# Performance work log

Hardware: AMD Instinct MI355X
Metric: run time of the kernel (lower is better)

## Reference

```python
import jax, jax.numpy as jnp
import numpy as np

N = 50000   # nodes
E = 800000  # edges
IN, HID, OUT, H = 128, 256, 128, 4
C1 = HID // H  # per-head channels for conv1/conv2
EPS_LN = 1e-5


def layer_norm(x, g, b):
    mu = x.mean(-1, keepdims=True)
    var = ((x - mu) ** 2).mean(-1, keepdims=True)
    return (x - mu) * jax.lax.rsqrt(var + EPS_LN) * g + b


def gatv2(x, src, dst, edge_attr, Wl, bl, Wr, br, We, att, bias, heads, ch, n):
    # PyG GATv2Conv (concat=True, negative_slope=0.2, share_weights=False)
    xl = (x @ Wl + bl).reshape(-1, heads, ch)   # [N,H,C] source transform
    xr = (x @ Wr + br).reshape(-1, heads, ch)   # [N,H,C] target transform
    e = (edge_attr @ We).reshape(-1, heads, ch) # [E,H,C] edge transform (no bias)
    m = jax.nn.leaky_relu(xl[src] + xr[dst] + e, 0.2)     # [E,H,C]
    logits = jnp.einsum('ehc,hc->eh', m, att)             # [E,H]
    mx = jax.ops.segment_max(logits, dst, num_segments=n) # segment softmax over dst
    a = jnp.exp(logits - mx[dst])
    denom = jax.ops.segment_sum(a, dst, num_segments=n)
    alpha = a / (denom[dst] + 1e-16)                      # [E,H]
    out = jax.ops.segment_sum(xl[src] * alpha[..., None], dst, num_segments=n)
    return out.reshape(-1, heads * ch) + bias


def setup_inputs() -> dict:
    key = jax.random.key(0)
    ks = jax.random.split(key, 24)
    s = 0.05
    inp = {
        'x': jax.random.normal(ks[0], (N, IN), jnp.float32),
        'edge_index': jax.random.randint(ks[1], (2, E), 0, N, jnp.int32),
        'edge_attr': jax.random.uniform(ks[2], (E, 1), jnp.float32),
        # conv1: in=IN, out per head=C1, heads=H
        'Wl1': jax.random.normal(ks[3], (IN, HID)) * s,  'bl1': jnp.zeros((HID,)),
        'Wr1': jax.random.normal(ks[4], (IN, HID)) * s,  'br1': jnp.zeros((HID,)),
        'We1': jax.random.normal(ks[5], (1, HID)) * s,
        'att1': jax.random.normal(ks[6], (H, C1)) * s,   'bo1': jnp.zeros((HID,)),
        'g1': jnp.ones((HID,)), 'be1': jnp.zeros((HID,)),
        # conv2: in=HID
        'Wl2': jax.random.normal(ks[7], (HID, HID)) * s, 'bl2': jnp.zeros((HID,)),
        'Wr2': jax.random.normal(ks[8], (HID, HID)) * s, 'br2': jnp.zeros((HID,)),
        'We2': jax.random.normal(ks[9], (1, HID)) * s,
        'att2': jax.random.normal(ks[10], (H, C1)) * s,  'bo2': jnp.zeros((HID,)),
        'g2': jnp.ones((HID,)), 'be2': jnp.zeros((HID,)),
        # conv3: heads=1, out=OUT
        'Wl3': jax.random.normal(ks[11], (HID, OUT)) * s, 'bl3': jnp.zeros((OUT,)),
        'Wr3': jax.random.normal(ks[12], (HID, OUT)) * s, 'br3': jnp.zeros((OUT,)),
        'We3': jax.random.normal(ks[13], (1, OUT)) * s,
        'att3': jax.random.normal(ks[14], (1, OUT)) * s,  'bo3': jnp.zeros((OUT,)),
        'g3': jnp.ones((OUT,)), 'be3': jnp.zeros((OUT,)),
    }
    return inp


def reference(x, edge_index, edge_attr,
              Wl1, bl1, Wr1, br1, We1, att1, bo1, g1, be1,
              Wl2, bl2, Wr2, br2, We2, att2, bo2, g2, be2,
              Wl3, bl3, Wr3, br3, We3, att3, bo3, g3, be3):
    src, dst = edge_index[0], edge_index[1]
    h = gatv2(x, src, dst, edge_attr, Wl1, bl1, Wr1, br1, We1, att1, bo1, H, C1, N)
    h = jax.nn.elu(layer_norm(h, g1, be1))  # dropout inactive at inference
    h = gatv2(h, src, dst, edge_attr, Wl2, bl2, Wr2, br2, We2, att2, bo2, H, C1, N)
    h = jax.nn.elu(layer_norm(h, g2, be2))
    h = gatv2(h, src, dst, edge_attr, Wl3, bl3, Wr3, br3, We3, att3, bo3, 1, OUT, N)
    return layer_norm(h, g3, be3)
```

## Files before the change

kernel.cpp:

```cpp
#include <hip/hip_runtime.h>
#include <cstdint>
#include <cstddef>

typedef unsigned short u16;
typedef __attribute__((ext_vector_type(8))) short short8v;
typedef __attribute__((ext_vector_type(4))) float f32x4;

#define IN_DIM 128
#define HID_DIM 256
#define OUT_DIM 128
#define HEADS 4

__device__ __forceinline__ float b2f(u16 v) {
    return __uint_as_float(((unsigned)v) << 16);
}
__device__ __forceinline__ u16 f2b(float f) {
    unsigned u = __float_as_uint(f);
    u += 0x7fffu + ((u >> 16) & 1u);
    return (u16)(u >> 16);
}


__global__ void count_k(const int* __restrict__ dst, int* __restrict__ counts, int ne) {
    int i = blockIdx.x * blockDim.x + threadIdx.x;
    if (i < ne) atomicAdd(&counts[dst[i]], 1);
}

__global__ __launch_bounds__(1024) void scan_k(const int* __restrict__ counts,
                                               int* __restrict__ offs,
                                               int* __restrict__ cursor, int n) {
    __shared__ int wtot[16];
    __shared__ int carry_s;
    int tid = threadIdx.x, wv = tid >> 6, ln = tid & 63;
    if (tid == 0) carry_s = 0;
    __syncthreads();
    for (int base = 0; base < n; base += 4096) {
        int i0 = base + tid * 4;
        int4 c4 = {0, 0, 0, 0};
        if (i0 + 3 < n) c4 = *(const int4*)(counts + i0);
        else {
            if (i0     < n) c4.x = counts[i0];
            if (i0 + 1 < n) c4.y = counts[i0 + 1];
            if (i0 + 2 < n) c4.z = counts[i0 + 2];
            if (i0 + 3 < n) c4.w = counts[i0 + 3];
        }
        int s0 = c4.x, s1 = s0 + c4.y, s2 = s1 + c4.z, s3 = s2 + c4.w;
        int v = s3;
#pragma unroll
        for (int o = 1; o < 64; o <<= 1) {
            int t = __shfl_up(v, o);
            if (ln >= o) v += t;
        }
        if (ln == 63) wtot[wv] = v;
        int wpref = v - s3;
        __syncthreads();
        if (wv == 0) {
            int w2 = (ln < 16) ? wtot[ln] : 0;
#pragma unroll
            for (int o = 1; o < 16; o <<= 1) {
                int t = __shfl_up(w2, o);
                if (ln >= o) w2 += t;
            }
            if (ln < 16) wtot[ln] = w2;
        }
        __syncthreads();
        int wbase = carry_s + (wv ? wtot[wv - 1] : 0);
        int ex0 = wbase + wpref;
        if (i0     < n) { offs[i0]     = ex0;      cursor[i0]     = ex0; }
        if (i0 + 1 < n) { offs[i0 + 1] = ex0 + s0; cursor[i0 + 1] = ex0 + s0; }
        if (i0 + 2 < n) { offs[i0 + 2] = ex0 + s1; cursor[i0 + 2] = ex0 + s1; }
        if (i0 + 3 < n) { offs[i0 + 3] = ex0 + s2; cursor[i0 + 3] = ex0 + s2; }
        __syncthreads();
        if (tid == 0) carry_s += wtot[15];
        __syncthreads();
    }
    if (threadIdx.x == 0) offs[n] = carry_s;
}

__global__ void fill_k(const int* __restrict__ src, const int* __restrict__ dst,
                       const float* __restrict__ ea, int* __restrict__ cursor,
                       int2* __restrict__ cedge, int ne) {
    int i = blockIdx.x * blockDim.x + threadIdx.x;
    if (i < ne) {
        int p = atomicAdd(&cursor[dst[i]], 1);
        int2 t;
        t.x = src[i];
        t.y = __float_as_int(ea[i]);
        cedge[p] = t;
    }
}


template <int KG>
__global__ void xpack_k(const float* __restrict__ X, short* __restrict__ Xp, int total) {
    int gid = blockIdx.x * blockDim.x + threadIdx.x;
    if (gid >= total) return;
    int lane = gid & 63;
    int kg = (gid >> 6) % KG;
    int rt = gid / (64 * KG);
    int row = rt * 16 + (lane & 15);
    int k0 = kg * 32 + ((lane >> 4) << 3);
    const float* src = X + (size_t)row * (KG * 32) + k0;
    short8v o;
#pragma unroll
    for (int j = 0; j < 8; j++) o[j] = (short)f2b(src[j]);
    ((short8v*)Xp)[gid] = o;
}

template <int K, int HOUT>
__global__ void packw_k(const float* __restrict__ Wl, const float* __restrict__ Wr,
                        short* __restrict__ Wp) {
    constexpr int KG = K / 32;
    int gid = blockIdx.x * blockDim.x + threadIdx.x;
    int lane = gid & 63;
    int kg = (gid >> 6) % KG;
    int nt = gid / (64 * KG);
    int col = nt * 16 + (lane & 15);
    int k0 = kg * 32 + ((lane >> 4) << 3);
    const float* Wsrc = (col < HOUT) ? Wl : Wr;
    int c2 = (col < HOUT) ? col : col - HOUT;
    short8v o;
#pragma unroll
    for (int j = 0; j < 8; j++) o[j] = (short)f2b(Wsrc[(size_t)(k0 + j) * HOUT + c2]);
    ((short8v*)Wp)[gid] = o;
}


template <int KG, int NT, int HOUT, int R>
__global__ __launch_bounds__(256) void gemm_mfma(
    const short* __restrict__ Xp, const short* __restrict__ Wp,
    const float* __restrict__ bl, const float* __restrict__ br,
    u16* __restrict__ XL, u16* __restrict__ XR, int nrt) {
    constexpr int NCG = NT / 8;
    int w = threadIdx.x >> 6, lane = threadIdx.x & 63;
    int cg = blockIdx.x % NCG;
    int rt0 = (blockIdx.x / NCG) * R;
    if (rt0 >= nrt) return;
    int rcnt = min(R, nrt - rt0);
    int nt0 = cg * 8 + w * 2;
    const short8v* wb = (const short8v*)Wp + lane;
    short8v wf0[KG], wf1[KG];
#pragma unroll
    for (int kg = 0; kg < KG; kg++) {
        wf0[kg] = wb[(size_t)(nt0 * KG + kg) * 64];
        wf1[kg] = wb[(size_t)((nt0 + 1) * KG + kg) * 64];
    }
    int colg0 = nt0 * 16 + ((lane >> 4) << 2);
    int colg1 = colg0 + 16;
    bool isr0 = colg0 >= HOUT;
    bool isr1 = colg1 >= HOUT;
    int cl0 = colg0 - (isr0 ? HOUT : 0);
    int cl1 = colg1 - (isr1 ? HOUT : 0);
    float4 bb0 = *(const float4*)((isr0 ? br : bl) + cl0);
    float4 bb1 = *(const float4*)((isr1 ? br : bl) + cl1);
    u16* ob0 = (isr0 ? XR : XL) + cl0;
    u16* ob1 = (isr1 ? XR : XL) + cl1;

    const short8v* xb = (const short8v*)Xp + (size_t)rt0 * KG * 64 + lane;
    for (int r = 0; r < rcnt; ++r) {
        f32x4 acc0 = {0.f, 0.f, 0.f, 0.f}, acc1 = {0.f, 0.f, 0.f, 0.f};
#pragma unroll
        for (int kg = 0; kg < KG; kg++) {
            short8v xf = xb[(size_t)(r * KG + kg) * 64];
            acc0 = __builtin_amdgcn_mfma_f32_16x16x32_bf16(wf0[kg], xf, acc0, 0, 0, 0);
            acc1 = __builtin_amdgcn_mfma_f32_16x16x32_bf16(wf1[kg], xf, acc1, 0, 0, 0);
        }
        size_t rowoff = (size_t)((rt0 + r) * 16 + (lane & 15)) * HOUT;
        ushort4 o0 = { f2b(acc0[0] + bb0.x), f2b(acc0[1] + bb0.y),
                       f2b(acc0[2] + bb0.z), f2b(acc0[3] + bb0.w) };
        *(ushort4*)(ob0 + rowoff) = o0;
        ushort4 o1 = { f2b(acc1[0] + bb1.x), f2b(acc1[1] + bb1.y),
                       f2b(acc1[2] + bb1.z), f2b(acc1[3] + bb1.w) };
        *(ushort4*)(ob1 + rowoff) = o1;
    }
}


__global__ __launch_bounds__(256) void gat_fused4(
    const int* __restrict__ offs, const int2* __restrict__ cedge,
    const float* __restrict__ We, const float* __restrict__ att,
    const u16* __restrict__ XL, const u16* __restrict__ XR,
    const float* __restrict__ bo, const float* __restrict__ g, const float* __restrict__ be,
    u16* __restrict__ hp, int n) {
    __shared__ int   sS[4][64];
    __shared__ float sEA[4][64];
    int tid = threadIdx.x;
    int w = tid >> 6;
    int lane = tid & 63;
    int node = blockIdx.x * 4 + w;
    int es = lane >> 5;
    int ls = lane & 31;
    int cabs = ls * 8;
    float xr[8], wev[8], atv[8];
    {
        short8v x8 = *(const short8v*)(XR + (size_t)node * 256 + cabs);
        float4 wA = *(const float4*)(We + cabs), wB = *(const float4*)(We + cabs + 4);
        float4 aA = *(const float4*)(att + cabs), aB = *(const float4*)(att + cabs + 4);
#pragma unroll
        for (int i = 0; i < 8; i++) xr[i] = b2f((u16)x8[i]);
        wev[0] = wA.x; wev[1] = wA.y; wev[2] = wA.z; wev[3] = wA.w;
        wev[4] = wB.x; wev[5] = wB.y; wev[6] = wB.z; wev[7] = wB.w;
        atv[0] = aA.x; atv[1] = aA.y; atv[2] = aA.z; atv[3] = aA.w;
        atv[4] = aB.x; atv[5] = aB.y; atv[6] = aB.z; atv[7] = aB.w;
    }
    int b0 = offs[node], eEnd = offs[node + 1];
    float dsum = 0.f;
    float acc[8];
#pragma unroll
    for (int i = 0; i < 8; i++) acc[i] = 0.f;
    for (int base = b0; base < eEnd; base += 64) {
        int cnt = min(64, eEnd - base);
        if (lane < cnt) {
            int2 t = cedge[base + lane];
            sS[w][lane] = t.x;
            sEA[w][lane] = __int_as_float(t.y);
        }
        short8v r0, r1, r2;
        float e0, e1f, e2;
        bool v0, v1, v2;
        {
            int j0 = es, j1 = es + 2, j2 = es + 4;
            v0 = j0 < cnt; v1 = j1 < cnt; v2 = j2 < cnt;
            int i0 = v0 ? j0 : 0, i1 = v1 ? j1 : 0, i2 = v2 ? j2 : 0;
            e0 = sEA[w][i0]; r0 = *(const short8v*)(XL + (size_t)sS[w][i0] * 256 + cabs);
            e1f = sEA[w][i1]; r1 = *(const short8v*)(XL + (size_t)sS[w][i1] * 256 + cabs);
            e2 = sEA[w][i2]; r2 = *(const short8v*)(XL + (size_t)sS[w][i2] * 256 + cabs);
        }
        for (int r = 0; r < cnt; r += 2) {
            short8v rc = r0; float ec = e0; bool vc = v0;
            r0 = r1; e0 = e1f; v0 = v1;
            r1 = r2; e1f = e2; v1 = v2;
            int jn = r + 6 + es;
            v2 = jn < cnt;
            int idx = v2 ? jn : 0;
            e2 = sEA[w][idx];
            r2 = *(const short8v*)(XL + (size_t)sS[w][idx] * 256 + cabs);
            float x[8];
#pragma unroll
            for (int i = 0; i < 8; i++) x[i] = b2f((u16)rc[i]);
            float p = 0.f;
#pragma unroll
            for (int i = 0; i < 8; i++) {
                float t = fmaf(ec, wev[i], x[i]) + xr[i];
                t = fmaxf(t, 0.2f * t);
                p += t * atv[i];
            }
            p += __shfl_xor(p, 1);
            p += __shfl_xor(p, 2);
            p += __shfl_xor(p, 4);
            float wv2 = vc ? __expf(p) : 0.f;
            dsum += wv2;
#pragma unroll
            for (int i = 0; i < 8; i++) acc[i] += wv2 * x[i];
        }
    }
    dsum += __shfl_xor(dsum, 32);
#pragma unroll
    for (int i = 0; i < 8; i++) acc[i] += __shfl_xor(acc[i], 32);
    float inv = 1.f / (dsum + 1e-16f);
    float4 bA = *(const float4*)(bo + cabs), bB = *(const float4*)(bo + cabs + 4);
    float v[8];
    v[0] = acc[0] * inv + bA.x; v[1] = acc[1] * inv + bA.y;
    v[2] = acc[2] * inv + bA.z; v[3] = acc[3] * inv + bA.w;
    v[4] = acc[4] * inv + bB.x; v[5] = acc[5] * inv + bB.y;
    v[6] = acc[6] * inv + bB.z; v[7] = acc[7] * inv + bB.w;
    float s1 = 0.f, s2 = 0.f;
#pragma unroll
    for (int i = 0; i < 8; i++) { s1 += v[i]; s2 += v[i] * v[i]; }
#pragma unroll
    for (int o = 16; o >= 1; o >>= 1) {
        s1 += __shfl_xor(s1, o);
        s2 += __shfl_xor(s2, o);
    }
    float mu = s1 / 256.f;
    float sinv = rsqrtf(s2 / 256.f - mu * mu + 1e-5f);
    if (es == 0) {
        float4 gA = *(const float4*)(g + cabs), gB = *(const float4*)(g + cabs + 4);
        float4 eA = *(const float4*)(be + cabs), eB = *(const float4*)(be + cabs + 4);
        float gg[8] = {gA.x, gA.y, gA.z, gA.w, gB.x, gB.y, gB.z, gB.w};
        float ee[8] = {eA.x, eA.y, eA.z, eA.w, eB.x, eB.y, eB.z, eB.w};
        short8v yv;
#pragma unroll
        for (int i = 0; i < 8; i++) {
            float y = (v[i] - mu) * sinv * gg[i] + ee[i];
            y = (y > 0.f) ? y : expm1f(y);
            yv[i] = (short)f2b(y);
        }
        int kg = cabs >> 5;
        int l = (node & 15) | (((cabs >> 3) & 3) << 4);
        size_t eoff = (((size_t)(node >> 4) * 8 + kg) * 64 + l) * 8;
        *(short8v*)(hp + eoff) = yv;
    }
}


__global__ __launch_bounds__(256) void gat_fused1(
    const int* __restrict__ offs, const int2* __restrict__ cedge,
    const float* __restrict__ We, const float* __restrict__ att,
    const u16* __restrict__ XL, const u16* __restrict__ XR,
    const float* __restrict__ bo, const float* __restrict__ g, const float* __restrict__ be,
    float* __restrict__ out, int n) {
    __shared__ int   sS[4][64];
    __shared__ float sEA[4][64];
    int tid = threadIdx.x;
    int w = tid >> 6;
    int lane = tid & 63;
    int node = blockIdx.x * 4 + w;
    int q = lane >> 4;
    int ls = lane & 15;
    int cb = ls * 8;
    float xr[8], wev[8], atv[8];
    {
        short8v x8 = *(const short8v*)(XR + (size_t)node * 128 + cb);
        float4 wA = *(const float4*)(We + cb), wB = *(const float4*)(We + cb + 4);
        float4 aA = *(const float4*)(att + cb), aB = *(const float4*)(att + cb + 4);
#pragma unroll
        for (int i = 0; i < 8; i++) xr[i] = b2f((u16)x8[i]);
        wev[0] = wA.x; wev[1] = wA.y; wev[2] = wA.z; wev[3] = wA.w;
        wev[4] = wB.x; wev[5] = wB.y; wev[6] = wB.z; wev[7] = wB.w;
        atv[0] = aA.x; atv[1] = aA.y; atv[2] = aA.z; atv[3] = aA.w;
        atv[4] = aB.x; atv[5] = aB.y; atv[6] = aB.z; atv[7] = aB.w;
    }
    int b0 = offs[node], eEnd = offs[node + 1];
    float dsum = 0.f;
    float acc[8];
#pragma unroll
    for (int i = 0; i < 8; i++) acc[i] = 0.f;
    for (int base = b0; base < eEnd; base += 64) {
        int cnt = min(64, eEnd - base);
        if (lane < cnt) {
            int2 t = cedge[base + lane];
            sS[w][lane] = t.x;
            sEA[w][lane] = __int_as_float(t.y);
        }
        short8v r0, r1, r2;
        float e0, e1f, e2;
        bool v0, v1, v2;
        {
            int j0 = q, j1 = q + 4, j2 = q + 8;
            v0 = j0 < cnt; v1 = j1 < cnt; v2 = j2 < cnt;
            int i0 = v0 ? j0 : 0, i1 = v1 ? j1 : 0, i2 = v2 ? j2 : 0;
            e0 = sEA[w][i0]; r0 = *(const short8v*)(XL + (size_t)sS[w][i0] * 128 + cb);
            e1f = sEA[w][i1]; r1 = *(const short8v*)(XL + (size_t)sS[w][i1] * 128 + cb);
            e2 = sEA[w][i2]; r2 = *(const short8v*)(XL + (size_t)sS[w][i2] * 128 + cb);
        }
        for (int r = 0; r < cnt; r += 4) {
            short8v rc = r0; float ec = e0; bool vc = v0;
            r0 = r1; e0 = e1f; v0 = v1;
            r1 = r2; e1f = e2; v1 = v2;
            int jn = r + 12 + q;
            v2 = jn < cnt;
            int idx = v2 ? jn : 0;
            e2 = sEA[w][idx];
            r2 = *(const short8v*)(XL + (size_t)sS[w][idx] * 128 + cb);
            float x[8];
#pragma unroll
            for (int i = 0; i < 8; i++) x[i] = b2f((u16)rc[i]);
            float p = 0.f;
#pragma unroll
            for (int i = 0; i < 8; i++) {
                float t = fmaf(ec, wev[i], x[i]) + xr[i];
                t = fmaxf(t, 0.2f * t);
                p += t * atv[i];
            }
            p += __shfl_xor(p, 1);
            p += __shfl_xor(p, 2);
            p += __shfl_xor(p, 4);
            p += __shfl_xor(p, 8);
            float wv2 = vc ? __expf(p) : 0.f;
            dsum += wv2;
#pragma unroll
            for (int i = 0; i < 8; i++) acc[i] += wv2 * x[i];
        }
    }
    dsum += __shfl_xor(dsum, 32);
    dsum += __shfl_xor(dsum, 16);
#pragma unroll
    for (int i = 0; i < 8; i++) {
        acc[i] += __shfl_xor(acc[i], 32);
        acc[i] += __shfl_xor(acc[i], 16);
    }
    float inv = 1.f / (dsum + 1e-16f);
    float4 bA = *(const float4*)(bo + cb), bB = *(const float4*)(bo + cb + 4);
    float v[8];
    v[0] = acc[0] * inv + bA.x; v[1] = acc[1] * inv + bA.y;
    v[2] = acc[2] * inv + bA.z; v[3] = acc[3] * inv + bA.w;
    v[4] = acc[4] * inv + bB.x; v[5] = acc[5] * inv + bB.y;
    v[6] = acc[6] * inv + bB.z; v[7] = acc[7] * inv + bB.w;
    float s1 = 0.f, s2 = 0.f;
#pragma unroll
    for (int i = 0; i < 8; i++) { s1 += v[i]; s2 += v[i] * v[i]; }
#pragma unroll
    for (int o = 8; o >= 1; o >>= 1) {
        s1 += __shfl_xor(s1, o);
        s2 += __shfl_xor(s2, o);
    }
    float mu = s1 / 128.f;
    float sinv = rsqrtf(s2 / 128.f - mu * mu + 1e-5f);
    if (q == 0) {
        float4 gA = *(const float4*)(g + cb), gB = *(const float4*)(g + cb + 4);
        float4 eA = *(const float4*)(be + cb), eB = *(const float4*)(be + cb + 4);
        float gg[8] = {gA.x, gA.y, gA.z, gA.w, gB.x, gB.y, gB.z, gB.w};
        float ee[8] = {eA.x, eA.y, eA.z, eA.w, eB.x, eB.y, eB.z, eB.w};
        float4 oA, oB;
        oA.x = (v[0] - mu) * sinv * gg[0] + ee[0];
        oA.y = (v[1] - mu) * sinv * gg[1] + ee[1];
        oA.z = (v[2] - mu) * sinv * gg[2] + ee[2];
        oA.w = (v[3] - mu) * sinv * gg[3] + ee[3];
        oB.x = (v[4] - mu) * sinv * gg[4] + ee[4];
        oB.y = (v[5] - mu) * sinv * gg[5] + ee[5];
        oB.z = (v[6] - mu) * sinv * gg[6] + ee[6];
        oB.w = (v[7] - mu) * sinv * gg[7] + ee[7];
        float* op = out + (size_t)node * 128 + cb;
        *(float4*)op = oA;
        *(float4*)(op + 4) = oB;
    }
}


extern "C" void kernel_launch(void* const* d_in, const int* in_sizes, int n_in,
                              void* d_out, int out_size, void* d_ws, size_t ws_size,
                              hipStream_t stream) {
    const float* x  = (const float*)d_in[0];
    const int*   ei = (const int*)d_in[1];
    const float* ea = (const float*)d_in[2];
    const float *Wl1 = (const float*)d_in[3],  *bl1 = (const float*)d_in[4];
    const float *Wr1 = (const float*)d_in[5],  *br1 = (const float*)d_in[6];
    const float *We1 = (const float*)d_in[7],  *att1 = (const float*)d_in[8];
    const float *bo1 = (const float*)d_in[9],  *g1 = (const float*)d_in[10], *be1 = (const float*)d_in[11];
    const float *Wl2 = (const float*)d_in[12], *bl2 = (const float*)d_in[13];
    const float *Wr2 = (const float*)d_in[14], *br2 = (const float*)d_in[15];
    const float *We2 = (const float*)d_in[16], *att2 = (const float*)d_in[17];
    const float *bo2 = (const float*)d_in[18], *g2 = (const float*)d_in[19], *be2 = (const float*)d_in[20];
    const float *Wl3 = (const float*)d_in[21], *bl3 = (const float*)d_in[22];
    const float *Wr3 = (const float*)d_in[23], *br3 = (const float*)d_in[24];
    const float *We3 = (const float*)d_in[25], *att3 = (const float*)d_in[26];
    const float *bo3 = (const float*)d_in[27], *g3 = (const float*)d_in[28], *be3 = (const float*)d_in[29];

    int n = in_sizes[0] / IN_DIM;
    int e = in_sizes[1] / 2;
    const int* srcv = ei;
    const int* dstv = ei + e;
    int nrt = n / 16;

    char* w = (char*)d_ws;
    size_t off = 0;
    auto take = [&](size_t bytes) -> void* {
        void* p = w + off;
        off = (off + bytes + 255) & ~(size_t)255;
        return p;
    };
    int*   counts = (int*)take((size_t)n * 4);
    int*   cursor = (int*)take((size_t)n * 4);
    int*   offs   = (int*)take((size_t)(n + 1) * 4);
    int2*  cedge  = (int2*)take((size_t)e * 8);
    u16*   XL     = (u16*)take((size_t)n * HID_DIM * 2);
    u16*   XR     = (u16*)take((size_t)n * HID_DIM * 2);
    short* xpack  = (short*)take((size_t)nrt * 4 * 64 * 8 * 2);
    short* hpack  = (short*)take((size_t)nrt * 8 * 64 * 8 * 2);
    short* wp1    = (short*)take((size_t)32 * 4 * 64 * 8 * 2);
    short* wp2    = (short*)take((size_t)32 * 8 * 64 * 8 * 2);
    short* wp3    = (short*)take((size_t)16 * 8 * 64 * 8 * 2);

    const int TPB = 256;
    int eb = (e + TPB - 1) / TPB;

    hipMemsetAsync(counts, 0, (size_t)n * 4, stream);
    count_k<<<eb, TPB, 0, stream>>>(dstv, counts, e);
    scan_k<<<1, 1024, 0, stream>>>(counts, offs, cursor, n);
    fill_k<<<eb, TPB, 0, stream>>>(srcv, dstv, ea, cursor, cedge, e);

    packw_k<IN_DIM,  HID_DIM><<<32 * 4 * 64 / TPB, TPB, 0, stream>>>(Wl1, Wr1, wp1);
    packw_k<HID_DIM, HID_DIM><<<32 * 8 * 64 / TPB, TPB, 0, stream>>>(Wl2, Wr2, wp2);
    packw_k<HID_DIM, OUT_DIM><<<16 * 8 * 64 / TPB, TPB, 0, stream>>>(Wl3, Wr3, wp3);
    int xtot = nrt * 4 * 64;
    xpack_k<4><<<(xtot + TPB - 1) / TPB, TPB, 0, stream>>>(x, xpack, xtot);

    gemm_mfma<4, 32, HID_DIM, 8><<<4 * ((nrt + 7) / 8), TPB, 0, stream>>>(
        xpack, wp1, bl1, br1, XL, XR, nrt);
    gat_fused4<<<n / 4, 256, 0, stream>>>(
        offs, cedge, We1, att1, XL, XR, bo1, g1, be1, (u16*)hpack, n);

    gemm_mfma<8, 32, HID_DIM, 8><<<4 * ((nrt + 7) / 8), TPB, 0, stream>>>(
        hpack, wp2, bl2, br2, XL, XR, nrt);
    gat_fused4<<<n / 4, 256, 0, stream>>>(
        offs, cedge, We2, att2, XL, XR, bo2, g2, be2, (u16*)hpack, n);

    gemm_mfma<8, 16, OUT_DIM, 4><<<2 * ((nrt + 3) / 4), TPB, 0, stream>>>(
        hpack, wp3, bl3, br3, XL, XR, nrt);
    gat_fused1<<<n / 4, 256, 0, stream>>>(
        offs, cedge, We3, att3, XL, XR, bo3, g3, be3, (float*)d_out, n);
}
```

Before: 436.7 us.

## Parallelize CSR offset scan across blocks and remap GEMM blocks per XCD

New measurement: 406.3 us. 7.0% less time.

```diff
diff --git a/kernel.cpp b/kernel.cpp
--- a/kernel.cpp
+++ b/kernel.cpp
@@ -26,55 +26,63 @@
     if (i < ne) atomicAdd(&counts[dst[i]], 1);
 }
 
-__global__ __launch_bounds__(1024) void scan_k(const int* __restrict__ counts,
-                                               int* __restrict__ offs,
-                                               int* __restrict__ cursor, int n) {
-    __shared__ int wtot[16];
-    __shared__ int carry_s;
-    int tid = threadIdx.x, wv = tid >> 6, ln = tid & 63;
-    if (tid == 0) carry_s = 0;
+__global__ __launch_bounds__(256) void scanA(const int* __restrict__ counts,
+                                             int* __restrict__ bsum, int n) {
+    __shared__ int ws[4];
+    int blk = blockIdx.x, tid = threadIdx.x;
+    int i0 = blk * 1024 + tid * 4;
+    int s = 0;
+#pragma unroll
+    for (int j = 0; j < 4; j++) { int i = i0 + j; if (i < n) s += counts[i]; }
+#pragma unroll
+    for (int o = 1; o < 64; o <<= 1) s += __shfl_xor(s, o);
+    int wv = tid >> 6, ln = tid & 63;
+    if (ln == 0) ws[wv] = s;
     __syncthreads();
-    for (int base = 0; base < n; base += 4096) {
-        int i0 = base + tid * 4;
-        int4 c4 = {0, 0, 0, 0};
-        if (i0 + 3 < n) c4 = *(const int4*)(counts + i0);
-        else {
-            if (i0     < n) c4.x = counts[i0];
-            if (i0 + 1 < n) c4.y = counts[i0 + 1];
-            if (i0 + 2 < n) c4.z = counts[i0 + 2];
-            if (i0 + 3 < n) c4.w = counts[i0 + 3];
-        }
-        int s0 = c4.x, s1 = s0 + c4.y, s2 = s1 + c4.z, s3 = s2 + c4.w;
-        int v = s3;
-#pragma unroll
-        for (int o = 1; o < 64; o <<= 1) {
-            int t = __shfl_up(v, o);
-            if (ln >= o) v += t;
-        }
-        if (ln == 63) wtot[wv] = v;
-        int wpref = v - s3;
-        __syncthreads();
-        if (wv == 0) {
-            int w2 = (ln < 16) ? wtot[ln] : 0;
-#pragma unroll
-            for (int o = 1; o < 16; o <<= 1) {
-                int t = __shfl_up(w2, o);
-                if (ln >= o) w2 += t;
-            }
-            if (ln < 16) wtot[ln] = w2;
-        }
-        __syncthreads();
-        int wbase = carry_s + (wv ? wtot[wv - 1] : 0);
-        int ex0 = wbase + wpref;
-        if (i0     < n) { offs[i0]     = ex0;      cursor[i0]     = ex0; }
-        if (i0 + 1 < n) { offs[i0 + 1] = ex0 + s0; cursor[i0 + 1] = ex0 + s0; }
-        if (i0 + 2 < n) { offs[i0 + 2] = ex0 + s1; cursor[i0 + 2] = ex0 + s1; }
-        if (i0 + 3 < n) { offs[i0 + 3] = ex0 + s2; cursor[i0 + 3] = ex0 + s2; }
-        __syncthreads();
-        if (tid == 0) carry_s += wtot[15];
-        __syncthreads();
-    }
-    if (threadIdx.x == 0) offs[n] = carry_s;
+    if (tid == 0) bsum[blk] = ws[0] + ws[1] + ws[2] + ws[3];
+}
+
+__global__ __launch_bounds__(64) void scanB(int* __restrict__ bsum, int nb) {
+    int ln = threadIdx.x;
+    int carry = 0;
+    for (int base = 0; base < nb; base += 64) {
+        int i = base + ln;
+        int v = (i < nb) ? bsum[i] : 0;
+        int x = v;
+#pragma unroll
+        for (int o = 1; o < 64; o <<= 1) { int t = __shfl_up(x, o); if (ln >= o) x += t; }
+        if (i < nb) bsum[i] = carry + x - v;
+        carry += __shfl(x, 63);
+    }
+}
+
+__global__ __launch_bounds__(256) void scanC(const int* __restrict__ counts,
+                                             const int* __restrict__ bsum,
+                                             int* __restrict__ offs, int* __restrict__ cursor,
+                                             int n) {
+    __shared__ int wtot[4];
+    int blk = blockIdx.x, tid = threadIdx.x, wv = tid >> 6, ln = tid & 63;
+    int i0 = blk * 1024 + tid * 4;
+    int c[4]; int s = 0;
+#pragma unroll
+    for (int j = 0; j < 4; j++) { int i = i0 + j; c[j] = (i < n) ? counts[i] : 0; s += c[j]; }
+    int x = s;
+#pragma unroll
+    for (int o = 1; o < 64; o <<= 1) { int t = __shfl_up(x, o); if (ln >= o) x += t; }
+    if (ln == 63) wtot[wv] = x;
+    int lpref = x - s;
+    __syncthreads();
+    int wbase = 0;
+    for (int i = 0; i < wv; i++) wbase += wtot[i];
+    int base = bsum[blk] + wbase + lpref;
+#pragma unroll
+    for (int j = 0; j < 4; j++) {
+        int i = i0 + j;
+        if (i < n) {
+            offs[i] = base; cursor[i] = base; base += c[j];
+            if (i == n - 1) offs[n] = base;
+        }
+    }
 }
 
 __global__ void fill_k(const int* __restrict__ src, const int* __restrict__ dst,
@@ -133,8 +141,11 @@
     u16* __restrict__ XL, u16* __restrict__ XR, int nrt) {
     constexpr int NCG = NT / 8;
     int w = threadIdx.x >> 6, lane = threadIdx.x & 63;
-    int cg = blockIdx.x % NCG;
-    int rt0 = (blockIdx.x / NCG) * R;
+    int xcd = blockIdx.x & 7;
+    int s = blockIdx.x >> 3;
+    int cg = s % NCG;
+    int rtg = xcd + 8 * (s / NCG);
+    int rt0 = rtg * R;
     if (rt0 >= nrt) return;
     int rcnt = min(R, nrt - rt0);
     int nt0 = cg * 8 + w * 2;
@@ -453,6 +464,7 @@
     int*   counts = (int*)take((size_t)n * 4);
     int*   cursor = (int*)take((size_t)n * 4);
     int*   offs   = (int*)take((size_t)(n + 1) * 4);
+    int*   bsum   = (int*)take(256 * 4);
     int2*  cedge  = (int2*)take((size_t)e * 8);
     u16*   XL     = (u16*)take((size_t)n * HID_DIM * 2);
     u16*   XR     = (u16*)take((size_t)n * HID_DIM * 2);
@@ -464,10 +476,13 @@
 
     const int TPB = 256;
     int eb = (e + TPB - 1) / TPB;
+    int nb = (n + 1023) / 1024;
 
     hipMemsetAsync(counts, 0, (size_t)n * 4, stream);
     count_k<<<eb, TPB, 0, stream>>>(dstv, counts, e);
-    scan_k<<<1, 1024, 0, stream>>>(counts, offs, cursor, n);
+    scanA<<<nb, TPB, 0, stream>>>(counts, bsum, n);
+    scanB<<<1, 64, 0, stream>>>(bsum, nb);
+    scanC<<<nb, TPB, 0, stream>>>(counts, bsum, offs, cursor, n);
     fill_k<<<eb, TPB, 0, stream>>>(srcv, dstv, ea, cursor, cedge, e);
 
     packw_k<IN_DIM,  HID_DIM><<<32 * 4 * 64 / TPB, TPB, 0, stream>>>(Wl1, Wr1, wp1);
@@ -476,17 +491,22 @@
     int xtot = nrt * 4 * 64;
     xpack_k<4><<<(xtot + TPB - 1) / TPB, TPB, 0, stream>>>(x, xpack, xtot);
 
-    gemm_mfma<4, 32, HID_DIM, 8><<<4 * ((nrt + 7) / 8), TPB, 0, stream>>>(
+    int nrtg8 = (nrt + 7) / 8;
+    int grid12 = 8 * ((nrtg8 + 7) / 8) * 4;
+    int nrtg4 = (nrt + 3) / 4;
+    int grid3 = 8 * ((nrtg4 + 7) / 8) * 2;
+
+    gemm_mfma<4, 32, HID_DIM, 8><<<grid12, TPB, 0, stream>>>(
         xpack, wp1, bl1, br1, XL, XR, nrt);
     gat_fused4<<<n / 4, 256, 0, stream>>>(
         offs, cedge, We1, att1, XL, XR, bo1, g1, be1, (u16*)hpack, n);
 
-    gemm_mfma<8, 32, HID_DIM, 8><<<4 * ((nrt + 7) / 8), TPB, 0, stream>>>(
+    gemm_mfma<8, 32, HID_DIM, 8><<<grid12, TPB, 0, stream>>>(
         hpack, wp2, bl2, br2, XL, XR, nrt);
     gat_fused4<<<n / 4, 256, 0, stream>>>(
         offs, cedge, We2, att2, XL, XR, bo2, g2, be2, (u16*)hpack, n);
 
-    gemm_mfma<8, 16, OUT_DIM, 4><<<2 * ((nrt + 3) / 4), TPB, 0, stream>>>(
+    gemm_mfma<8, 16, OUT_DIM, 4><<<grid3, TPB, 0, stream>>>(
         hpack, wp3, bl3, br3, XL, XR, nrt);
     gat_fused1<<<n / 4, 256, 0, stream>>>(
         offs, cedge, We3, att3, XL, XR, bo3, g3, be3, (float*)d_out, n);
```
